# Kernel tuning notes

Hardware: AMD Instinct MI355X
Metric: run time of the kernel (lower is better)

The kernel has to match this reference:

```python
import jax, jax.numpy as jnp
import numpy as np

GAMMA = 0.95        # gamma_lemma: persistence decay per cycle (eq. 12.1)
KAPPA = 0.1         # kappa_interfere: lateral interference strength (eq. 12.3)
T_STEPS = 50        # t_lemma_steps: integration window before selection (eq. 12.2)
FLOOR = 1e-6        # confidence_floor for peak-to-average ratio

B, N_CONCEPTS, N_LEMMAS = 4096, 1024, 512


def setup_inputs() -> dict:
    key = jax.random.key(0)
    k1, k2 = jax.random.split(key, 2)
    # kernel boundary hands in a normalized concept distribution
    c_raw = jax.random.uniform(k1, (B, N_CONCEPTS), dtype=jnp.float32)
    c_lex = c_raw / jnp.sum(c_raw, axis=-1, keepdims=True)
    # TiedSubstrate W_C_to_L: (out_dim=n_lemmas, in_dim=n_concepts)
    W = jax.random.normal(k2, (N_LEMMAS, N_CONCEPTS), dtype=jnp.float32) / np.sqrt(N_CONCEPTS)
    # persistent lemma activation buffer a_lemma, zero at reset
    a0 = jnp.zeros((B, N_LEMMAS), dtype=jnp.float32)
    return {"c_lex": c_lex, "W": W, "a0": a0}


def reference(c_lex, W, a0):
    """Integrate lemma activations for T_STEPS cycles, then select.

    Per cycle (eq. 12.1 + 12.3):
      a <- gamma * a + c_lex @ W^T            # decay + concept->lemma drive
      a <- a - kappa * (sum_j a_j - a)        # lateral interference from other lemmas
      a <- max(a, 0)                          # rectify activations
    Selection (eq. 12.2): argmax over lemmas; confidence = peak / max(mean, floor).
    """
    def step(a, _):
        a = GAMMA * a + jnp.einsum('bc,lc->bl', c_lex, W)   # (B, n_lemmas)
        a = a - KAPPA * (jnp.sum(a, axis=-1, keepdims=True) - a)
        a = jnp.maximum(a, 0.0)
        return a, None

    a, _ = jax.lax.scan(step, a0, None, length=T_STEPS)
    peak = jnp.max(a, axis=-1)
    mean = jnp.mean(a, axis=-1)
    confidence = peak / jnp.maximum(mean, FLOOR)
    selected = jnp.argmax(a, axis=-1)
    return a, selected, confidence
```

## Files before the change

kernel.cpp:

```cpp
#include <hip/hip_runtime.h>
#include <hip/hip_bf16.h>

#define BATCH 4096
#define NC    1024
#define NL    512
#define TSTEPS 50
#define GAMMA_C 0.95f
#define KAPPA_C 0.1f
#define FLOOR_C 1e-6f

typedef __attribute__((ext_vector_type(8))) short short8;
typedef __attribute__((ext_vector_type(4))) float f32x4;

__device__ inline void split_bf16(float x, unsigned short& h, unsigned short& l) {
    unsigned u = __float_as_uint(x);
    unsigned rh = u + 0x7FFFu + ((u >> 16) & 1u);
    h = (unsigned short)(rh >> 16);
    float hf = __uint_as_float((unsigned)h << 16);
    float r = x - hf;
    unsigned v = __float_as_uint(r);
    unsigned rl = v + 0x7FFFu + ((v >> 16) & 1u);
    l = (unsigned short)(rl >> 16);
}

__global__ __launch_bounds__(256)
void convert_split(const float* __restrict__ A, const float* __restrict__ W,
                   unsigned short* __restrict__ Ahi, unsigned short* __restrict__ Alo,
                   unsigned short* __restrict__ Whi, unsigned short* __restrict__ Wlo) {
    const int chunk = blockIdx.x * 256 + threadIdx.x;
    const int fidx  = chunk * 4;
    const float* src;
    unsigned short *dh, *dl;
    if (fidx < BATCH * NC) {
        src = A + fidx; dh = Ahi + fidx; dl = Alo + fidx;
    } else {
        const int o = fidx - BATCH * NC;
        src = W + o; dh = Whi + o; dl = Wlo + o;
    }
    const float4 v = *(const float4*)src;
    ushort4 h4, l4;
    split_bf16(v.x, h4.x, l4.x);
    split_bf16(v.y, h4.y, l4.y);
    split_bf16(v.z, h4.z, l4.z);
    split_bf16(v.w, h4.w, l4.w);
    *(ushort4*)dh = h4;
    *(ushort4*)dl = l4;
}

#define TM 128
#define TN 128
#define GK 32
#define LDT 40

__global__ __launch_bounds__(512)
void gemm_bf16x2(const unsigned short* __restrict__ Ahi, const unsigned short* __restrict__ Alo,
                 const unsigned short* __restrict__ Whi, const unsigned short* __restrict__ Wlo,
                 float* __restrict__ D0, float* __restrict__ D1) {
    __shared__ unsigned short AsH[TM * LDT];
    __shared__ unsigned short AsL[TM * LDT];
    __shared__ unsigned short BsH[TN * LDT];
    __shared__ unsigned short BsL[TN * LDT];

    const int tid = threadIdx.x;
    const int m0 = blockIdx.x * TM;
    const int n0 = blockIdx.y * TN;
    const int kb = blockIdx.z * (NC / 2);
    float* __restrict__ D = blockIdx.z ? D1 : D0;

    const int srow = tid >> 2;
    const int skc  = (tid & 3) * 8;

    const unsigned short* gAh = Ahi + (size_t)(m0 + srow) * NC + kb + skc;
    const unsigned short* gAl = Alo + (size_t)(m0 + srow) * NC + kb + skc;
    const unsigned short* gBh = Whi + (size_t)(n0 + srow) * NC + kb + skc;
    const unsigned short* gBl = Wlo + (size_t)(n0 + srow) * NC + kb + skc;

    unsigned short* wAh = AsH + srow * LDT + skc;
    unsigned short* wAl = AsL + srow * LDT + skc;
    unsigned short* wBh = BsH + srow * LDT + skc;
    unsigned short* wBl = BsL + srow * LDT + skc;

    const int lane = tid & 63;
    const int w    = tid >> 6;
    const int mw   = (w >> 2) * 64;
    const int nw   = (w & 3) * 32;
    const int sr   = lane & 15;
    const int quad = lane >> 4;

    const unsigned short* rAh = AsH + (mw + sr) * LDT + quad * 8;
    const unsigned short* rAl = AsL + (mw + sr) * LDT + quad * 8;
    const unsigned short* rBh = BsH + (nw + sr) * LDT + quad * 8;
    const unsigned short* rBl = BsL + (nw + sr) * LDT + quad * 8;

    f32x4 acc[4][2];
    #pragma unroll
    for (int i = 0; i < 4; ++i)
        #pragma unroll
        for (int j = 0; j < 2; ++j)
            acc[i][j] = (f32x4){0.f, 0.f, 0.f, 0.f};

    short8 pAh = *(const short8*)gAh;
    short8 pAl = *(const short8*)gAl;
    short8 pBh = *(const short8*)gBh;
    short8 pBl = *(const short8*)gBl;

    for (int kt = 0; kt < NC / 2; kt += GK) {
        *(short8*)wAh = pAh;
        *(short8*)wAl = pAl;
        *(short8*)wBh = pBh;
        *(short8*)wBl = pBl;
        __syncthreads();

        const int kn = (kt + GK < NC / 2) ? kt + GK : 0;
        pAh = *(const short8*)(gAh + kn);
        pAl = *(const short8*)(gAl + kn);
        pBh = *(const short8*)(gBh + kn);
        pBl = *(const short8*)(gBl + kn);

        short8 afh[4], afl[4], bfh[2], bfl[2];
        #pragma unroll
        for (int mi = 0; mi < 4; ++mi) {
            afh[mi] = *(const short8*)(rAh + mi * 16 * LDT);
            afl[mi] = *(const short8*)(rAl + mi * 16 * LDT);
        }
        #pragma unroll
        for (int ni = 0; ni < 2; ++ni) {
            bfh[ni] = *(const short8*)(rBh + ni * 16 * LDT);
            bfl[ni] = *(const short8*)(rBl + ni * 16 * LDT);
        }

        #pragma unroll
        for (int mi = 0; mi < 4; ++mi) {
            #pragma unroll
            for (int ni = 0; ni < 2; ++ni) {
                acc[mi][ni] = __builtin_amdgcn_mfma_f32_16x16x32_bf16(
                    afh[mi], bfh[ni], acc[mi][ni], 0, 0, 0);
                acc[mi][ni] = __builtin_amdgcn_mfma_f32_16x16x32_bf16(
                    afh[mi], bfl[ni], acc[mi][ni], 0, 0, 0);
                acc[mi][ni] = __builtin_amdgcn_mfma_f32_16x16x32_bf16(
                    afl[mi], bfh[ni], acc[mi][ni], 0, 0, 0);
            }
        }
        __syncthreads();
    }

    #pragma unroll
    for (int mi = 0; mi < 4; ++mi) {
        #pragma unroll
        for (int ni = 0; ni < 2; ++ni) {
            const int col = n0 + nw + ni * 16 + sr;
            #pragma unroll
            for (int r = 0; r < 4; ++r) {
                const int row = m0 + mw + mi * 16 + quad * 4 + r;
                D[(size_t)row * NL + col] = acc[mi][ni][r];
            }
        }
    }
}

__global__ __launch_bounds__(256)
void iterate_select(const float* __restrict__ D0, float* a_out,
                    float* sel_out, float* conf_out) {
    const int lane = threadIdx.x & 63;
    const int wave = threadIdx.x >> 6;
    const int sub  = lane & 31;
    const int grp  = lane >> 5;
    const int row  = blockIdx.x * 8 + wave * 2 + grp;

    float d[16];
    {
        const float4* p0 = (const float4*)(D0    + (size_t)row * NL + sub * 16);
        const float4* p1 = (const float4*)(a_out + (size_t)row * NL + sub * 16);
        #pragma unroll
        for (int p = 0; p < 4; ++p) {
            const float4 v0 = p0[p];
            const float4 v1 = p1[p];
            d[4 * p + 0] = v0.x + v1.x;
            d[4 * p + 1] = v0.y + v1.y;
            d[4 * p + 2] = v0.z + v1.z;
            d[4 * p + 3] = v0.w + v1.w;
        }
    }

    float a[16];
    #pragma unroll
    for (int j = 0; j < 16; ++j) a[j] = 0.f;

    const float K1 = 1.0f + KAPPA_C;

    for (int t = 0; t < TSTEPS; ++t) {
        #pragma unroll
        for (int j = 0; j < 16; ++j) a[j] = fmaf(GAMMA_C, a[j], d[j]);

        float t8[8], t4[4], t2[2];
        #pragma unroll
        for (int j = 0; j < 8; ++j) t8[j] = a[j] + a[j + 8];
        #pragma unroll
        for (int j = 0; j < 4; ++j) t4[j] = t8[j] + t8[j + 4];
        t2[0] = t4[0] + t4[2]; t2[1] = t4[1] + t4[3];
        float S = t2[0] + t2[1];

        S += __shfl_xor(S, 1, 64);
        S += __shfl_xor(S, 2, 64);
        S += __shfl_xor(S, 4, 64);
        S += __shfl_xor(S, 8, 64);
        S += __shfl_xor(S, 16, 64);

        const float h = -KAPPA_C * S;
        #pragma unroll
        for (int j = 0; j < 16; ++j) {
            const float v = fmaf(K1, a[j], h);
            a[j] = v > 0.f ? v : 0.f;
        }
    }

    float m8[8], m4[4], s8[8], s4[4];
    #pragma unroll
    for (int j = 0; j < 8; ++j) { m8[j] = fmaxf(a[j], a[j + 8]); s8[j] = a[j] + a[j + 8]; }
    #pragma unroll
    for (int j = 0; j < 4; ++j) { m4[j] = fmaxf(m8[j], m8[j + 4]); s4[j] = s8[j] + s8[j + 4]; }
    float peak = fmaxf(fmaxf(m4[0], m4[1]), fmaxf(m4[2], m4[3]));
    float ssum = (s4[0] + s4[1]) + (s4[2] + s4[3]);

    peak = fmaxf(peak, __shfl_xor(peak, 1, 64));
    peak = fmaxf(peak, __shfl_xor(peak, 2, 64));
    peak = fmaxf(peak, __shfl_xor(peak, 4, 64));
    peak = fmaxf(peak, __shfl_xor(peak, 8, 64));
    peak = fmaxf(peak, __shfl_xor(peak, 16, 64));
    ssum += __shfl_xor(ssum, 1, 64);
    ssum += __shfl_xor(ssum, 2, 64);
    ssum += __shfl_xor(ssum, 4, 64);
    ssum += __shfl_xor(ssum, 8, 64);
    ssum += __shfl_xor(ssum, 16, 64);

    const float mean = ssum * (1.0f / (float)NL);
    const float conf = peak / fmaxf(mean, FLOOR_C);

    int idx = 0x7fffffff;
    #pragma unroll
    for (int j = 0; j < 16; ++j)
        if (a[j] == peak) idx = min(idx, sub * 16 + j);
    idx = min(idx, __shfl_xor(idx, 1, 64));
    idx = min(idx, __shfl_xor(idx, 2, 64));
    idx = min(idx, __shfl_xor(idx, 4, 64));
    idx = min(idx, __shfl_xor(idx, 8, 64));
    idx = min(idx, __shfl_xor(idx, 16, 64));

    float4* ar = (float4*)(a_out + (size_t)row * NL + sub * 16);
    #pragma unroll
    for (int p = 0; p < 4; ++p) {
        float4 v;
        v.x = a[4 * p + 0]; v.y = a[4 * p + 1]; v.z = a[4 * p + 2]; v.w = a[4 * p + 3];
        ar[p] = v;
    }

    if (sub == 0) {
        if (sel_out)  sel_out[row]  = (float)idx;
        if (conf_out) conf_out[row] = conf;
    }
}

extern "C" void kernel_launch(void* const* d_in, const int* in_sizes, int n_in,
                              void* d_out, int out_size, void* d_ws, size_t ws_size,
                              hipStream_t stream) {
    const float* c_lex = (const float*)d_in[0];
    const float* W     = (const float*)d_in[1];

    float* D0 = (float*)d_ws;
    unsigned short* Ahi = (unsigned short*)(D0 + BATCH * NL);
    unsigned short* Alo = Ahi + (size_t)BATCH * NC;
    unsigned short* Whi = Alo + (size_t)BATCH * NC;
    unsigned short* Wlo = Whi + (size_t)NL * NC;

    float* a_out = (float*)d_out;
    float* sel   = nullptr;
    float* conf  = nullptr;
    const int base = BATCH * NL;
    if (out_size >= base + 2 * BATCH) {
        sel  = a_out + base;
        conf = a_out + base + BATCH;
    } else if (out_size >= base + BATCH) {
        conf = a_out + base;
    }

    convert_split<<<dim3(4608), 256, 0, stream>>>(c_lex, W, Ahi, Alo, Whi, Wlo);

    gemm_bf16x2<<<dim3(BATCH / TM, NL / TN, 2), 512, 0, stream>>>(
        Ahi, Alo, Whi, Wlo, D0, a_out);

    iterate_select<<<dim3(BATCH / 8), 256, 0, stream>>>(D0, a_out, sel, conf);
}
```

Baseline: 114.6 us.

## Widen GEMM N-tile to 256 and split K four ways into workspace partials

Doubles the GEMM block's N tile to 256, so each wave computes a 64x64 sub-tile with 16 accumulators and reuses its A fragments across more MFMAs. To keep the grid at 256 blocks, K is now split four ways, and all partial sums go to a workspace buffer; the output buffer is no longer used as scratch. The iterate kernel is templated on the split count and sums the four partials. This raises operand reuse per LDS load, at the cost of more register pressure, a larger workspace, and extra global traffic for the partials.

```diff
diff --git a/kernel.cpp b/kernel.cpp
--- a/kernel.cpp
+++ b/kernel.cpp
@@ -48,14 +48,14 @@
 }
 
 #define TM 128
-#define TN 128
+#define TN 256
 #define GK 32
 #define LDT 40
 
 __global__ __launch_bounds__(512)
 void gemm_bf16x2(const unsigned short* __restrict__ Ahi, const unsigned short* __restrict__ Alo,
                  const unsigned short* __restrict__ Whi, const unsigned short* __restrict__ Wlo,
-                 float* __restrict__ D0, float* __restrict__ D1) {
+                 float* __restrict__ Dp, int kPerSplit) {
     __shared__ unsigned short AsH[TM * LDT];
     __shared__ unsigned short AsL[TM * LDT];
     __shared__ unsigned short BsH[TN * LDT];
@@ -64,26 +64,27 @@
     const int tid = threadIdx.x;
     const int m0 = blockIdx.x * TM;
     const int n0 = blockIdx.y * TN;
-    const int kb = blockIdx.z * (NC / 2);
-    float* __restrict__ D = blockIdx.z ? D1 : D0;
-
-    const int srow = tid >> 2;
-    const int skc  = (tid & 3) * 8;
-
-    const unsigned short* gAh = Ahi + (size_t)(m0 + srow) * NC + kb + skc;
-    const unsigned short* gAl = Alo + (size_t)(m0 + srow) * NC + kb + skc;
-    const unsigned short* gBh = Whi + (size_t)(n0 + srow) * NC + kb + skc;
-    const unsigned short* gBl = Wlo + (size_t)(n0 + srow) * NC + kb + skc;
-
-    unsigned short* wAh = AsH + srow * LDT + skc;
-    unsigned short* wAl = AsL + srow * LDT + skc;
-    unsigned short* wBh = BsH + srow * LDT + skc;
-    unsigned short* wBl = BsL + srow * LDT + skc;
+    const int kb = blockIdx.z * kPerSplit;
+
+    const int srA = tid >> 2;
+    const int kcA = (tid & 3) * 8;
+    const int srB = tid >> 1;
+    const int kcB = (tid & 1) * 16;
+
+    const unsigned short* gAh = Ahi + (size_t)(m0 + srA) * NC + kb + kcA;
+    const unsigned short* gAl = Alo + (size_t)(m0 + srA) * NC + kb + kcA;
+    const unsigned short* gBh = Whi + (size_t)(n0 + srB) * NC + kb + kcB;
+    const unsigned short* gBl = Wlo + (size_t)(n0 + srB) * NC + kb + kcB;
+
+    unsigned short* wAh = AsH + srA * LDT + kcA;
+    unsigned short* wAl = AsL + srA * LDT + kcA;
+    unsigned short* wBh = BsH + srB * LDT + kcB;
+    unsigned short* wBl = BsL + srB * LDT + kcB;
 
     const int lane = tid & 63;
     const int w    = tid >> 6;
     const int mw   = (w >> 2) * 64;
-    const int nw   = (w & 3) * 32;
+    const int nw   = (w & 3) * 64;
     const int sr   = lane & 15;
     const int quad = lane >> 4;
 
@@ -92,39 +93,45 @@
     const unsigned short* rBh = BsH + (nw + sr) * LDT + quad * 8;
     const unsigned short* rBl = BsL + (nw + sr) * LDT + quad * 8;
 
-    f32x4 acc[4][2];
+    f32x4 acc[4][4];
     #pragma unroll
     for (int i = 0; i < 4; ++i)
         #pragma unroll
-        for (int j = 0; j < 2; ++j)
+        for (int j = 0; j < 4; ++j)
             acc[i][j] = (f32x4){0.f, 0.f, 0.f, 0.f};
 
     short8 pAh = *(const short8*)gAh;
     short8 pAl = *(const short8*)gAl;
-    short8 pBh = *(const short8*)gBh;
-    short8 pBl = *(const short8*)gBl;
-
-    for (int kt = 0; kt < NC / 2; kt += GK) {
+    short8 pBh0 = *(const short8*)gBh;
+    short8 pBh1 = *(const short8*)(gBh + 8);
+    short8 pBl0 = *(const short8*)gBl;
+    short8 pBl1 = *(const short8*)(gBl + 8);
+
+    for (int kt = 0; kt < kPerSplit; kt += GK) {
         *(short8*)wAh = pAh;
         *(short8*)wAl = pAl;
-        *(short8*)wBh = pBh;
-        *(short8*)wBl = pBl;
+        *(short8*)wBh = pBh0;
+        *(short8*)(wBh + 8) = pBh1;
+        *(short8*)wBl = pBl0;
+        *(short8*)(wBl + 8) = pBl1;
         __syncthreads();
 
-        const int kn = (kt + GK < NC / 2) ? kt + GK : 0;
+        const int kn = (kt + GK < kPerSplit) ? kt + GK : 0;
         pAh = *(const short8*)(gAh + kn);
         pAl = *(const short8*)(gAl + kn);
-        pBh = *(const short8*)(gBh + kn);
-        pBl = *(const short8*)(gBl + kn);
-
-        short8 afh[4], afl[4], bfh[2], bfl[2];
+        pBh0 = *(const short8*)(gBh + kn);
+        pBh1 = *(const short8*)(gBh + kn + 8);
+        pBl0 = *(const short8*)(gBl + kn);
+        pBl1 = *(const short8*)(gBl + kn + 8);
+
+        short8 afh[4], afl[4], bfh[4], bfl[4];
         #pragma unroll
         for (int mi = 0; mi < 4; ++mi) {
             afh[mi] = *(const short8*)(rAh + mi * 16 * LDT);
             afl[mi] = *(const short8*)(rAl + mi * 16 * LDT);
         }
         #pragma unroll
-        for (int ni = 0; ni < 2; ++ni) {
+        for (int ni = 0; ni < 4; ++ni) {
             bfh[ni] = *(const short8*)(rBh + ni * 16 * LDT);
             bfl[ni] = *(const short8*)(rBl + ni * 16 * LDT);
         }
@@ -132,7 +139,7 @@
         #pragma unroll
         for (int mi = 0; mi < 4; ++mi) {
             #pragma unroll
-            for (int ni = 0; ni < 2; ++ni) {
+            for (int ni = 0; ni < 4; ++ni) {
                 acc[mi][ni] = __builtin_amdgcn_mfma_f32_16x16x32_bf16(
                     afh[mi], bfh[ni], acc[mi][ni], 0, 0, 0);
                 acc[mi][ni] = __builtin_amdgcn_mfma_f32_16x16x32_bf16(
@@ -144,23 +151,26 @@
         __syncthreads();
     }
 
+    float* Dz = Dp + (size_t)blockIdx.z * BATCH * NL;
     #pragma unroll
     for (int mi = 0; mi < 4; ++mi) {
         #pragma unroll
-        for (int ni = 0; ni < 2; ++ni) {
+        for (int ni = 0; ni < 4; ++ni) {
             const int col = n0 + nw + ni * 16 + sr;
             #pragma unroll
             for (int r = 0; r < 4; ++r) {
                 const int row = m0 + mw + mi * 16 + quad * 4 + r;
-                D[(size_t)row * NL + col] = acc[mi][ni][r];
+                Dz[(size_t)row * NL + col] = acc[mi][ni][r];
             }
         }
     }
 }
 
+template<int SK>
 __global__ __launch_bounds__(256)
-void iterate_select(const float* __restrict__ D0, float* a_out,
-                    float* sel_out, float* conf_out) {
+void iterate_select(const float* __restrict__ Dp,
+                    float* __restrict__ a_out,
+                    float* __restrict__ sel_out, float* __restrict__ conf_out) {
     const int lane = threadIdx.x & 63;
     const int wave = threadIdx.x >> 6;
     const int sub  = lane & 31;
@@ -169,16 +179,22 @@
 
     float d[16];
     {
-        const float4* p0 = (const float4*)(D0    + (size_t)row * NL + sub * 16);
-        const float4* p1 = (const float4*)(a_out + (size_t)row * NL + sub * 16);
+        const float4* p0 = (const float4*)(Dp + (size_t)row * NL + sub * 16);
         #pragma unroll
         for (int p = 0; p < 4; ++p) {
-            const float4 v0 = p0[p];
-            const float4 v1 = p1[p];
-            d[4 * p + 0] = v0.x + v1.x;
-            d[4 * p + 1] = v0.y + v1.y;
-            d[4 * p + 2] = v0.z + v1.z;
-            d[4 * p + 3] = v0.w + v1.w;
+            const float4 v = p0[p];
+            d[4 * p + 0] = v.x; d[4 * p + 1] = v.y; d[4 * p + 2] = v.z; d[4 * p + 3] = v.w;
+        }
+        #pragma unroll
+        for (int s = 1; s < SK; ++s) {
+            const float4* ps = (const float4*)(Dp + (size_t)s * BATCH * NL
+                                               + (size_t)row * NL + sub * 16);
+            #pragma unroll
+            for (int p = 0; p < 4; ++p) {
+                const float4 v = ps[p];
+                d[4 * p + 0] += v.x; d[4 * p + 1] += v.y;
+                d[4 * p + 2] += v.z; d[4 * p + 3] += v.w;
+            }
         }
     }
 
@@ -266,8 +282,8 @@
     const float* c_lex = (const float*)d_in[0];
     const float* W     = (const float*)d_in[1];
 
-    float* D0 = (float*)d_ws;
-    unsigned short* Ahi = (unsigned short*)(D0 + BATCH * NL);
+    float* D = (float*)d_ws;
+    unsigned short* Ahi = (unsigned short*)(D + 4ull * BATCH * NL);
     unsigned short* Alo = Ahi + (size_t)BATCH * NC;
     unsigned short* Whi = Alo + (size_t)BATCH * NC;
     unsigned short* Wlo = Whi + (size_t)NL * NC;
@@ -285,8 +301,9 @@
 
     convert_split<<<dim3(4608), 256, 0, stream>>>(c_lex, W, Ahi, Alo, Whi, Wlo);
 
-    gemm_bf16x2<<<dim3(BATCH / TM, NL / TN, 2), 512, 0, stream>>>(
-        Ahi, Alo, Whi, Wlo, D0, a_out);
-
-    iterate_select<<<dim3(BATCH / 8), 256, 0, stream>>>(D0, a_out, sel, conf);
-}
+    const int kPerSplit = NC / 4;
+    gemm_bf16x2<<<dim3(BATCH / TM, NL / TN, 4), 512, 0, stream>>>(
+        Ahi, Alo, Whi, Wlo, D, kPerSplit);
+
+    iterate_select<4><<<dim3(BATCH / 8), 256, 0, stream>>>(D, a_out, sel, conf);
+}
```

Measured after the change: 115.1 us. About the same (+0.4%).
